# Kernel optimization log

Measured on AMD Instinct MI355X. Metric: run time of the kernel, lower is better.

The kernel has to match this reference:

```python
import jax, jax.numpy as jnp
import numpy as np
import math

B, T, C, H = 4, 2048, 1024, 16
D = C // H  # head dim = 64


def setup_inputs() -> dict:
    key = jax.random.key(0)
    ks = jax.random.split(key, 5)
    scale = 0.02
    x = jax.random.normal(ks[0], (B, T, C), dtype=jnp.float32)
    # torch nn.Linear(n_embd, 3*n_embd): weight [3C, C]; we store transposed [C, 3C]
    W_kqv = jax.random.normal(ks[1], (C, 3 * C), dtype=jnp.float32) * scale
    b_kqv = jnp.zeros((3 * C,), dtype=jnp.float32)
    W_proj = jax.random.normal(ks[2], (C, C), dtype=jnp.float32) * scale
    b_proj = jnp.zeros((C,), dtype=jnp.float32)
    padding_mask = jnp.ones((B, T), dtype=jnp.int32)  # 1 = valid token
    return {"x": x, "W_kqv": W_kqv, "b_kqv": b_kqv, "W_proj": W_proj,
            "b_proj": b_proj, "padding_mask": padding_mask}


def reference(x, W_kqv, b_kqv, W_proj, b_proj, padding_mask):
    Bx, Tx, Cx = x.shape
    kqv = x @ W_kqv + b_kqv                      # [B,T,3C]
    # original splits as k, q, v (in that order)
    k, q, v = jnp.split(kqv, 3, axis=2)
    def heads(t):
        return t.reshape(Bx, Tx, H, D).transpose(0, 2, 1, 3)  # [B,H,T,D]
    k, q, v = heads(k), heads(q), heads(v)
    att = jnp.einsum('bhqd,bhkd->bhqk', q, k) * (1.0 / math.sqrt(D))  # [B,H,T,T]
    causal = jnp.tril(jnp.ones((Tx, Tx), dtype=bool))[None, None]     # [1,1,T,T]
    valid = causal & (padding_mask[:, None, None, :] != 0)            # [B,1,T,T] broadcast
    neg_inf = jnp.finfo(att.dtype).min
    att = jnp.where(valid, att, neg_inf)
    att = jax.nn.softmax(att, axis=-1)
    y = jnp.einsum('bhqk,bhkd->bhqd', att, v)    # [B,H,T,D]
    y = y.transpose(0, 2, 1, 3).reshape(Bx, Tx, Cx)
    return y @ W_proj + b_proj
```

## Files before the change

### kernel.cpp

```cpp
#include <hip/hip_runtime.h>


typedef short bf16x8 __attribute__((ext_vector_type(8)));
typedef float floatx4 __attribute__((ext_vector_type(4)));

#define MFMA16(a, b, c) __builtin_amdgcn_mfma_f32_16x16x32_bf16(a, b, c, 0, 0, 0)

#define ASYNC_COPY16(gp, lp)                                                   \
  __builtin_amdgcn_global_load_lds(                                            \
      (__attribute__((address_space(1))) void*)(gp),                           \
      (__attribute__((address_space(3))) void*)(lp), 16, 0, 0)

#define DRAIN_VMCNT() asm volatile("s_waitcnt vmcnt(0)" ::: "memory")
#define WAIT_VMCNT6() asm volatile("s_waitcnt vmcnt(6)" ::: "memory")

#if defined(__has_builtin)
#if __has_builtin(__builtin_amdgcn_exp2f)
#define EXP2(x) __builtin_amdgcn_exp2f(x)
#endif
#endif
#ifndef EXP2
#define EXP2(x) exp2f(x)
#endif

__device__ __forceinline__ short f2bf(float f) {
  union { float f; unsigned u; } c;
  c.f = f;
  unsigned r = c.u + 0x7fffu + ((c.u >> 16) & 1u);
  return (short)(r >> 16);
}

__global__ __launch_bounds__(256) void cvt_f32_bf16(const float* __restrict__ in,
                                                    short* __restrict__ out) {
  int i = (blockIdx.x * 256 + threadIdx.x) * 4;
  float4 v = *(const float4*)&in[i];
  short4 o;
  o.x = f2bf(v.x); o.y = f2bf(v.y); o.z = f2bf(v.z); o.w = f2bf(v.w);
  *(short4*)&out[i] = o;
}

__global__ __launch_bounds__(256) void pmb_kernel(const int* __restrict__ pm,
                                                  float* __restrict__ pmbf) {
  int i = blockIdx.x * 256 + threadIdx.x;
  pmbf[i] = pm[i] ? 0.0f : -3.0e38f;
}

__global__ __launch_bounds__(256) void transpose_cvt_tiled(const float* __restrict__ in,
                                                           short* __restrict__ out,
                                                           int N) {
  __shared__ float buf[64][65];
  const int t = threadIdx.x;
  const int k0 = blockIdx.y * 64, n0 = blockIdx.x * 64;
#pragma unroll
  for (int i = 0; i < 4; ++i) {
    int s = t + i * 256;
    int row = s >> 4, c4 = (s & 15) * 4;
    float4 v = *(const float4*)&in[(size_t)(k0 + row) * N + n0 + c4];
    buf[row][c4] = v.x; buf[row][c4 + 1] = v.y;
    buf[row][c4 + 2] = v.z; buf[row][c4 + 3] = v.w;
  }
  __syncthreads();
#pragma unroll
  for (int i = 0; i < 2; ++i) {
    int u = t + i * 256;
    int rn = u >> 3, ch = (u & 7) * 8;
    short tmp[8];
#pragma unroll
    for (int j = 0; j < 8; ++j) tmp[j] = f2bf(buf[ch + j][rn]);
    *(uint4*)&out[(size_t)(n0 + rn) * 1024 + k0 + ch] = *(uint4*)tmp;
  }
}

template <int MODE>
__global__ __launch_bounds__(512, 2) void gemm_ph256(const short* __restrict__ A,
                                                     const short* __restrict__ Bt,
                                                     const float* __restrict__ bias,
                                                     void* __restrict__ Cout,
                                                     int M, int N, int K) {
  __shared__ short smem[73728];
  const int tid = threadIdx.x;
  const int lane = tid & 63;
  const int wv = tid >> 6;
  const int l15 = lane & 15, quad = lane >> 4;
  const int xr = l15 & 7;
  const int m0 = blockIdx.y * 128, n0 = blockIdx.x * 256;
  const int wm = (wv >> 2) * 64, wn = (wv & 3) * 64;
  const int NT = K >> 6;

  floatx4 acc[4][4] = {};

#define STAGE_A(kt, bs, j)                                                     \
  { int c_ = (j) * 512 + tid;                                                  \
    int r_ = c_ >> 3, ch_ = (c_ & 7) ^ (r_ & 7);                               \
    ASYNC_COPY16(&A[(size_t)(m0 + r_) * K + (kt) * 64 + ch_ * 8],              \
                 &smem[(bs) * 8192 + c_ * 8]); }
#define STAGE_B(kt, bs, j)                                                     \
  { int c_ = (j) * 512 + tid;                                                  \
    int r_ = c_ >> 3, ch_ = (c_ & 7) ^ (r_ & 7);                               \
    ASYNC_COPY16(&Bt[(size_t)(n0 + r_) * K + (kt) * 64 + ch_ * 8],             \
                 &smem[24576 + (bs) * 16384 + c_ * 8]); }

  STAGE_A(0, 0, 0); STAGE_A(0, 0, 1);
  STAGE_B(0, 0, 0); STAGE_B(0, 0, 1); STAGE_B(0, 0, 2); STAGE_B(0, 0, 3);
  STAGE_A(1, 1, 0); STAGE_A(1, 1, 1);
  STAGE_B(1, 1, 0); STAGE_B(1, 1, 1); STAGE_B(1, 1, 2); STAGE_B(1, 1, 3);
  WAIT_VMCNT6();
  __builtin_amdgcn_s_barrier();

  int cur = 0, nxt = 2;
  for (int kt = 0; kt < NT; ++kt) {
    const bool st = (kt + 2 < NT);
    const short* Asr = &smem[cur * 8192];
    const short* Bsr = &smem[24576 + cur * 16384];

    if (st) { STAGE_A(kt + 2, nxt, 0); STAGE_A(kt + 2, nxt, 1); STAGE_B(kt + 2, nxt, 0); }
    bf16x8 af[4][2], bf0[2][2];
#pragma unroll
    for (int mi = 0; mi < 4; ++mi)
#pragma unroll
      for (int s = 0; s < 2; ++s)
        af[mi][s] = *(const bf16x8*)
            &Asr[(wm + mi * 16 + l15) * 64 + (((s * 4 + quad) ^ xr) * 8)];
#pragma unroll
    for (int nj = 0; nj < 2; ++nj)
#pragma unroll
      for (int s = 0; s < 2; ++s)
        bf0[nj][s] = *(const bf16x8*)
            &Bsr[(wn + nj * 16 + l15) * 64 + (((s * 4 + quad) ^ xr) * 8)];
    __builtin_amdgcn_s_setprio(1);
#pragma unroll
    for (int s = 0; s < 2; ++s)
#pragma unroll
      for (int mi = 0; mi < 4; ++mi)
#pragma unroll
        for (int nj = 0; nj < 2; ++nj)
          acc[mi][nj] = MFMA16(af[mi][s], bf0[nj][s], acc[mi][nj]);
    __builtin_amdgcn_s_setprio(0);
    __builtin_amdgcn_s_barrier();

    if (st) { STAGE_B(kt + 2, nxt, 1); STAGE_B(kt + 2, nxt, 2); STAGE_B(kt + 2, nxt, 3); }
    bf16x8 bf1[2][2];
#pragma unroll
    for (int nj = 0; nj < 2; ++nj)
#pragma unroll
      for (int s = 0; s < 2; ++s)
        bf1[nj][s] = *(const bf16x8*)
            &Bsr[(wn + (2 + nj) * 16 + l15) * 64 + (((s * 4 + quad) ^ xr) * 8)];
    __builtin_amdgcn_s_setprio(1);
#pragma unroll
    for (int s = 0; s < 2; ++s)
#pragma unroll
      for (int mi = 0; mi < 4; ++mi)
#pragma unroll
        for (int nj = 0; nj < 2; ++nj)
          acc[mi][2 + nj] = MFMA16(af[mi][s], bf1[nj][s], acc[mi][2 + nj]);
    __builtin_amdgcn_s_setprio(0);
    if (st) { WAIT_VMCNT6(); } else { DRAIN_VMCNT(); }
    __builtin_amdgcn_s_barrier();
    cur = (cur == 2) ? 0 : cur + 1;
    nxt = (nxt == 2) ? 0 : nxt + 1;
  }
#undef STAGE_A
#undef STAGE_B

  if (MODE == 0) {
    float* outf = (float*)Cout;
#pragma unroll
    for (int ni = 0; ni < 4; ++ni) {
      int col = n0 + wn + ni * 16 + l15;
      float bv = bias[col];
#pragma unroll
      for (int mi = 0; mi < 4; ++mi) {
#pragma unroll
        for (int rr = 0; rr < 4; ++rr) {
          int row = m0 + wm + mi * 16 + quad * 4 + rr;
          outf[(size_t)row * N + col] = acc[mi][ni][rr] + bv;
        }
      }
    }
  } else {
    short* outs = (short*)Cout;
    const size_t QOFF = (size_t)64 * 2048 * 64;
    const int sec = n0 >> 10;
    short* Es = smem;
    if (sec < 2) {
#pragma unroll
      for (int ni = 0; ni < 4; ++ni) {
        int c = wn + ni * 16 + l15;
        float bv = bias[n0 + c];
#pragma unroll
        for (int mi = 0; mi < 4; ++mi) {
          int r0 = wm + mi * 16 + quad * 4;
#pragma unroll
          for (int rr = 0; rr < 4; ++rr) {
            int r = r0 + rr;
            Es[r * 256 + (c ^ (((r >> 2) & 3) << 4))] = f2bf(acc[mi][ni][rr] + bv);
          }
        }
      }
    } else {
#pragma unroll
      for (int ni = 0; ni < 4; ++ni) {
        int c = wn + ni * 16 + l15;
        float bv = bias[n0 + c];
#pragma unroll
        for (int mi = 0; mi < 4; ++mi) {
          int r0 = wm + mi * 16 + quad * 4;
#pragma unroll
          for (int rr = 0; rr < 4; ++rr) {
            int r = r0 + rr;
            Es[c * 128 + (r ^ ((c & 7) << 3))] = f2bf(acc[mi][ni][rr] + bv);
          }
        }
      }
    }
    __syncthreads();
    if (sec < 2) {
#pragma unroll
      for (int jj = 0; jj < 8; ++jj) {
        int idx = jj * 512 + tid;
        int rr2 = idx >> 5;
        int cc2 = (idx & 31) * 8;
        uint4 v = *(const uint4*)&Es[rr2 * 256 + (cc2 ^ (((rr2 >> 2) & 3) << 4))];
        int colg = n0 + cc2;
        int hh = (colg >> 6) & 15, dd = colg & 63;
        int row = m0 + rr2, bb = row >> 11, tt = row & 2047;
        *(uint4*)(outs + (size_t)sec * QOFF +
                  (((size_t)(bb * 16 + hh) * 2048 + tt) * 64 + dd)) = v;
      }
    } else {
#pragma unroll
      for (int jj = 0; jj < 8; ++jj) {
        int idx = jj * 512 + tid;
        int cd = idx >> 4;
        int rb = (idx & 15) * 8;
        uint4 v = *(const uint4*)&Es[cd * 128 + (rb ^ ((cd & 7) << 3))];
        int colg = n0 + cd;
        int hh = (colg >> 6) & 15, dd = colg & 63;
        int trow = m0 + rb, bb = trow >> 11, tt = trow & 2047;
        *(uint4*)(outs + 2 * QOFF +
                  ((size_t)(bb * 16 + hh) * 64 + dd) * 2048 + tt) = v;
      }
    }
  }
}

__global__ __launch_bounds__(256, 3) void attn_flash8(const short* __restrict__ Qd,
                                                      const short* __restrict__ Kd,
                                                      const short* __restrict__ Vd,
                                                      const float* __restrict__ pmbf,
                                                      short* __restrict__ y) {
  constexpr int T = 2048, C = 1024;
  __shared__ short Ks[2][64 * 64];
  __shared__ short Vs[2][64 * 64];
  __shared__ short Ps[4][32][64];

  const int tid = threadIdx.x;
  const int lane = tid & 63, w = tid >> 6;
  const int l15 = lane & 15, quad = lane >> 4;
  const int xr = l15 & 7;
  const int lin = blockIdx.x;
  const int qb = 15 - (lin >> 6);
  const int bh = lin & 63;
  const int b = bh >> 4, h = bh & 15;
  const short* Qb = Qd + (size_t)bh * T * 64;
  const short* Kb = Kd + (size_t)bh * T * 64;
  const short* Vb = Vd + (size_t)bh * 64 * T;
  const float* pmb = &pmbf[b * T];
  const int q0 = qb * 128;
  const int nt = (q0 >> 6) + 2;

  const float SCALE2 = 0.18033688011112042f;

#define STAGE_KV(t, buf)                                                       \
  {                                                                            \
    const short* ksrc_ = Kb + (size_t)((t) * 64) * 64;                         \
    const short* vsrc_ = Vb + (t) * 64;                                        \
    _Pragma("unroll")                                                          \
    for (int j_ = 0; j_ < 2; ++j_) {                                           \
      int c_ = j_ * 256 + tid;                                                 \
      int r_ = c_ >> 3, cc_ = (c_ & 7) ^ (r_ & 7);                             \
      ASYNC_COPY16(ksrc_ + r_ * 64 + cc_ * 8, &Ks[buf][c_ * 8]);               \
      ASYNC_COPY16(vsrc_ + (size_t)r_ * T + cc_ * 8, &Vs[buf][c_ * 8]);        \
    }                                                                          \
  }

  bf16x8 qf[2][2];
#pragma unroll
  for (int mi = 0; mi < 2; ++mi) {
    const short* qp = Qb + (size_t)(q0 + w * 32 + mi * 16 + l15) * 64;
    qf[mi][0] = *(const bf16x8*)&qp[quad * 8];
    qf[mi][1] = *(const bf16x8*)&qp[32 + quad * 8];
  }

  floatx4 Oacc[2][4] = {};
  float lpart[2] = {};

  STAGE_KV(0, 0);
  DRAIN_VMCNT();
  __syncthreads();

  int cur = 0;
#pragma unroll 1
  for (int t = 0; t < nt; ++t) {
    const int k0 = t * 64;
    if (t + 1 < nt) STAGE_KV(t + 1, cur ^ 1);

    floatx4 Sacc[2][4] = {};
#pragma unroll
    for (int s = 0; s < 2; ++s) {
#pragma unroll
      for (int n4 = 0; n4 < 4; ++n4) {
        bf16x8 bK = *(const bf16x8*)
            &Ks[cur][(n4 * 16 + l15) * 64 + (((s * 4 + quad) ^ xr) * 8)];
        Sacc[0][n4] = MFMA16(bK, qf[0][s], Sacc[0][n4]);
        Sacc[1][n4] = MFMA16(bK, qf[1][s], Sacc[1][n4]);
      }
    }

    if (k0 < q0) {
#pragma unroll
      for (int n4 = 0; n4 < 4; ++n4) {
        floatx4 pb4 = *(const floatx4*)&pmb[k0 + n4 * 16 + quad * 4];
#pragma unroll
        for (int mi = 0; mi < 2; ++mi) {
          float p[4];
#pragma unroll
          for (int rr = 0; rr < 4; ++rr) {
            p[rr] = EXP2(fmaf(Sacc[mi][n4][rr], SCALE2, pb4[rr]));
            lpart[mi] += p[rr];
          }
          unsigned lo, hi;
          asm("v_cvt_pk_bf16_f32 %0, %1, %2" : "=v"(lo) : "v"(p[0]), "v"(p[1]));
          asm("v_cvt_pk_bf16_f32 %0, %1, %2" : "=v"(hi) : "v"(p[2]), "v"(p[3]));
          uint2 pk; pk.x = lo; pk.y = hi;
          *(uint2*)&Ps[w][mi * 16 + l15]
                      [((n4 * 2 + (quad >> 1)) ^ xr) * 8 + (quad & 1) * 4] = pk;
        }
      }
    } else {
#pragma unroll
      for (int n4 = 0; n4 < 4; ++n4) {
        floatx4 pb4 = *(const floatx4*)&pmb[k0 + n4 * 16 + quad * 4];
        const int colb = n4 * 16 + quad * 4;
#pragma unroll
        for (int mi = 0; mi < 2; ++mi) {
          const int rowb = (q0 - k0) + w * 32 + mi * 16 + l15;
          float p[4];
#pragma unroll
          for (int rr = 0; rr < 4; ++rr) {
            float v = EXP2(fmaf(Sacc[mi][n4][rr], SCALE2, pb4[rr]));
            if (colb + rr > rowb) v = 0.f;
            p[rr] = v;
            lpart[mi] += v;
          }
          unsigned lo, hi;
          asm("v_cvt_pk_bf16_f32 %0, %1, %2" : "=v"(lo) : "v"(p[0]), "v"(p[1]));
          asm("v_cvt_pk_bf16_f32 %0, %1, %2" : "=v"(hi) : "v"(p[2]), "v"(p[3]));
          uint2 pk; pk.x = lo; pk.y = hi;
          *(uint2*)&Ps[w][mi * 16 + l15]
                      [((n4 * 2 + (quad >> 1)) ^ xr) * 8 + (quad & 1) * 4] = pk;
        }
      }
    }

#pragma unroll
    for (int ks2 = 0; ks2 < 2; ++ks2) {
      const int pco = (((ks2 * 4 + quad) ^ xr) * 8);
      bf16x8 ap0 = *(const bf16x8*)&Ps[w][l15][pco];
      bf16x8 ap1 = *(const bf16x8*)&Ps[w][16 + l15][pco];
#pragma unroll
      for (int nd = 0; nd < 4; ++nd) {
        bf16x8 bV = *(const bf16x8*)
            &Vs[cur][(nd * 16 + l15) * 64 + (((ks2 * 4 + quad) ^ xr) * 8)];
        Oacc[0][nd] = MFMA16(ap0, bV, Oacc[0][nd]);
        Oacc[1][nd] = MFMA16(ap1, bV, Oacc[1][nd]);
      }
    }

    DRAIN_VMCNT();
    __syncthreads();
    cur ^= 1;
  }
#undef STAGE_KV

#pragma unroll
  for (int mi = 0; mi < 2; ++mi) {
    float s = lpart[mi];
    s += __shfl_xor(s, 16, 64);
    s += __shfl_xor(s, 32, 64);
    float inv_l[4];
#pragma unroll
    for (int rr = 0; rr < 4; ++rr)
      inv_l[rr] = 1.0f / __shfl(s, quad * 4 + rr, 16);
#pragma unroll
    for (int n = 0; n < 4; ++n) {
      int dcol = n * 16 + l15;
#pragma unroll
      for (int rr = 0; rr < 4; ++rr) {
        int rowq = q0 + w * 32 + mi * 16 + quad * 4 + rr;
        y[((size_t)(b * T + rowq)) * C + h * 64 + dcol] =
            f2bf(Oacc[mi][n][rr] * inv_l[rr]);
      }
    }
  }
}

extern "C" void kernel_launch(void* const* d_in, const int* in_sizes, int n_in,
                              void* d_out, int out_size, void* d_ws, size_t ws_size,
                              hipStream_t stream) {
  constexpr int B = 4, T = 2048, C = 1024;
  constexpr int M = B * T;
  constexpr int N1 = 3 * C;

  const float* x      = (const float*)d_in[0];
  const float* W_kqv  = (const float*)d_in[1];
  const float* b_kqv  = (const float*)d_in[2];
  const float* W_proj = (const float*)d_in[3];
  const float* b_proj = (const float*)d_in[4];
  const int*   pmask  = (const int*)d_in[5];
  float* out = (float*)d_out;

  const size_t QOFF = (size_t)64 * T * 64;

  short* xb     = (short*)d_ws;
  short* Wkqvt  = xb + (size_t)M * C;
  short* Wprojt = Wkqvt + (size_t)N1 * C;
  short* qkv    = Wprojt + (size_t)C * C;
  float* pmbf   = (float*)(qkv + 3 * QOFF);
  short* yb     = xb;

  short* Kd = qkv;
  short* Qd = qkv + QOFF;
  short* Vd = qkv + 2 * QOFF;

  cvt_f32_bf16<<<(M * C) / (256 * 4), 256, 0, stream>>>(x, xb);
  transpose_cvt_tiled<<<dim3(N1 / 64, 16), 256, 0, stream>>>(W_kqv, Wkqvt, N1);
  transpose_cvt_tiled<<<dim3(C / 64, 16), 256, 0, stream>>>(W_proj, Wprojt, C);
  pmb_kernel<<<(B * T) / 256, 256, 0, stream>>>(pmask, pmbf);

  gemm_ph256<2><<<dim3(N1 / 256, M / 128), 512, 0, stream>>>(xb, Wkqvt, b_kqv, Kd, M, N1, C);

  attn_flash8<<<dim3(1024), 256, 0, stream>>>(Qd, Kd, Vd, pmbf, yb);

  gemm_ph256<0><<<dim3(C / 256, M / 128), 512, 0, stream>>>(yb, Wprojt, b_proj, out, M, C, C);
}
```

Baseline: 252.6 us.

## Split GEMM k-step into four quadrant phases and fuse prep kernels

```diff
diff --git a/kernel.cpp b/kernel.cpp
--- a/kernel.cpp
+++ b/kernel.cpp
@@ -39,18 +39,19 @@
   *(short4*)&out[i] = o;
 }
 
-__global__ __launch_bounds__(256) void pmb_kernel(const int* __restrict__ pm,
-                                                  float* __restrict__ pmbf) {
-  int i = blockIdx.x * 256 + threadIdx.x;
-  pmbf[i] = pm[i] ? 0.0f : -3.0e38f;
-}
-
-__global__ __launch_bounds__(256) void transpose_cvt_tiled(const float* __restrict__ in,
-                                                           short* __restrict__ out,
-                                                           int N) {
+__global__ __launch_bounds__(256) void transpose_cvt2(const float* __restrict__ inA,
+                                                      short* __restrict__ outA,
+                                                      const float* __restrict__ inB,
+                                                      short* __restrict__ outB) {
   __shared__ float buf[64][65];
   const int t = threadIdx.x;
-  const int k0 = blockIdx.y * 64, n0 = blockIdx.x * 64;
+  const int bx = blockIdx.x;
+  const float* in;
+  short* out;
+  int N, n0;
+  if (bx < 48) { in = inA; out = outA; N = 3072; n0 = bx * 64; }
+  else         { in = inB; out = outB; N = 1024; n0 = (bx - 48) * 64; }
+  const int k0 = blockIdx.y * 64;
 #pragma unroll
   for (int i = 0; i < 4; ++i) {
     int s = t + i * 256;
@@ -112,48 +113,77 @@
     const bool st = (kt + 2 < NT);
     const short* Asr = &smem[cur * 8192];
     const short* Bsr = &smem[24576 + cur * 16384];
-
-    if (st) { STAGE_A(kt + 2, nxt, 0); STAGE_A(kt + 2, nxt, 1); STAGE_B(kt + 2, nxt, 0); }
-    bf16x8 af[4][2], bf0[2][2];
-#pragma unroll
-    for (int mi = 0; mi < 4; ++mi)
+    bf16x8 aA[2][2], aB[2][2], bA[2][2], bB[2][2];
+
+    if (st) { STAGE_A(kt + 2, nxt, 0); STAGE_A(kt + 2, nxt, 1); }
+#pragma unroll
+    for (int mi = 0; mi < 2; ++mi)
 #pragma unroll
       for (int s = 0; s < 2; ++s)
-        af[mi][s] = *(const bf16x8*)
+        aA[mi][s] = *(const bf16x8*)
             &Asr[(wm + mi * 16 + l15) * 64 + (((s * 4 + quad) ^ xr) * 8)];
 #pragma unroll
     for (int nj = 0; nj < 2; ++nj)
 #pragma unroll
       for (int s = 0; s < 2; ++s)
-        bf0[nj][s] = *(const bf16x8*)
+        bA[nj][s] = *(const bf16x8*)
             &Bsr[(wn + nj * 16 + l15) * 64 + (((s * 4 + quad) ^ xr) * 8)];
     __builtin_amdgcn_s_setprio(1);
 #pragma unroll
     for (int s = 0; s < 2; ++s)
 #pragma unroll
-      for (int mi = 0; mi < 4; ++mi)
+      for (int mi = 0; mi < 2; ++mi)
 #pragma unroll
         for (int nj = 0; nj < 2; ++nj)
-          acc[mi][nj] = MFMA16(af[mi][s], bf0[nj][s], acc[mi][nj]);
+          acc[mi][nj] = MFMA16(aA[mi][s], bA[nj][s], acc[mi][nj]);
     __builtin_amdgcn_s_setprio(0);
     __builtin_amdgcn_s_barrier();
 
-    if (st) { STAGE_B(kt + 2, nxt, 1); STAGE_B(kt + 2, nxt, 2); STAGE_B(kt + 2, nxt, 3); }
-    bf16x8 bf1[2][2];
+    if (st) { STAGE_B(kt + 2, nxt, 0); STAGE_B(kt + 2, nxt, 1); }
+#pragma unroll
+    for (int mi = 0; mi < 2; ++mi)
+#pragma unroll
+      for (int s = 0; s < 2; ++s)
+        aB[mi][s] = *(const bf16x8*)
+            &Asr[(wm + (2 + mi) * 16 + l15) * 64 + (((s * 4 + quad) ^ xr) * 8)];
+    __builtin_amdgcn_s_setprio(1);
+#pragma unroll
+    for (int s = 0; s < 2; ++s)
+#pragma unroll
+      for (int mi = 0; mi < 2; ++mi)
+#pragma unroll
+        for (int nj = 0; nj < 2; ++nj)
+          acc[2 + mi][nj] = MFMA16(aB[mi][s], bA[nj][s], acc[2 + mi][nj]);
+    __builtin_amdgcn_s_setprio(0);
+    __builtin_amdgcn_s_barrier();
+
+    if (st) { STAGE_B(kt + 2, nxt, 2); }
 #pragma unroll
     for (int nj = 0; nj < 2; ++nj)
 #pragma unroll
       for (int s = 0; s < 2; ++s)
-        bf1[nj][s] = *(const bf16x8*)
+        bB[nj][s] = *(const bf16x8*)
             &Bsr[(wn + (2 + nj) * 16 + l15) * 64 + (((s * 4 + quad) ^ xr) * 8)];
     __builtin_amdgcn_s_setprio(1);
 #pragma unroll
     for (int s = 0; s < 2; ++s)
 #pragma unroll
-      for (int mi = 0; mi < 4; ++mi)
+      for (int mi = 0; mi < 2; ++mi)
 #pragma unroll
         for (int nj = 0; nj < 2; ++nj)
-          acc[mi][2 + nj] = MFMA16(af[mi][s], bf1[nj][s], acc[mi][2 + nj]);
+          acc[mi][2 + nj] = MFMA16(aA[mi][s], bB[nj][s], acc[mi][2 + nj]);
+    __builtin_amdgcn_s_setprio(0);
+    __builtin_amdgcn_s_barrier();
+
+    if (st) { STAGE_B(kt + 2, nxt, 3); }
+    __builtin_amdgcn_s_setprio(1);
+#pragma unroll
+    for (int s = 0; s < 2; ++s)
+#pragma unroll
+      for (int mi = 0; mi < 2; ++mi)
+#pragma unroll
+        for (int nj = 0; nj < 2; ++nj)
+          acc[2 + mi][2 + nj] = MFMA16(aB[mi][s], bB[nj][s], acc[2 + mi][2 + nj]);
     __builtin_amdgcn_s_setprio(0);
     if (st) { WAIT_VMCNT6(); } else { DRAIN_VMCNT(); }
     __builtin_amdgcn_s_barrier();
@@ -248,7 +278,7 @@
 __global__ __launch_bounds__(256, 3) void attn_flash8(const short* __restrict__ Qd,
                                                       const short* __restrict__ Kd,
                                                       const short* __restrict__ Vd,
-                                                      const float* __restrict__ pmbf,
+                                                      const int* __restrict__ pmask,
                                                       short* __restrict__ y) {
   constexpr int T = 2048, C = 1024;
   __shared__ short Ks[2][64 * 64];
@@ -266,7 +296,7 @@
   const short* Qb = Qd + (size_t)bh * T * 64;
   const short* Kb = Kd + (size_t)bh * T * 64;
   const short* Vb = Vd + (size_t)bh * 64 * T;
-  const float* pmb = &pmbf[b * T];
+  const int* pmi = &pmask[b * T];
   const int q0 = qb * 128;
   const int nt = (q0 >> 6) + 2;
 
@@ -321,13 +351,18 @@
     if (k0 < q0) {
 #pragma unroll
       for (int n4 = 0; n4 < 4; ++n4) {
-        floatx4 pb4 = *(const floatx4*)&pmb[k0 + n4 * 16 + quad * 4];
+        int4 pm4 = *(const int4*)&pmi[k0 + n4 * 16 + quad * 4];
+        float pb[4];
+        pb[0] = pm4.x ? 0.0f : -3.0e38f;
+        pb[1] = pm4.y ? 0.0f : -3.0e38f;
+        pb[2] = pm4.z ? 0.0f : -3.0e38f;
+        pb[3] = pm4.w ? 0.0f : -3.0e38f;
 #pragma unroll
         for (int mi = 0; mi < 2; ++mi) {
           float p[4];
 #pragma unroll
           for (int rr = 0; rr < 4; ++rr) {
-            p[rr] = EXP2(fmaf(Sacc[mi][n4][rr], SCALE2, pb4[rr]));
+            p[rr] = EXP2(fmaf(Sacc[mi][n4][rr], SCALE2, pb[rr]));
             lpart[mi] += p[rr];
           }
           unsigned lo, hi;
@@ -341,7 +376,12 @@
     } else {
 #pragma unroll
       for (int n4 = 0; n4 < 4; ++n4) {
-        floatx4 pb4 = *(const floatx4*)&pmb[k0 + n4 * 16 + quad * 4];
+        int4 pm4 = *(const int4*)&pmi[k0 + n4 * 16 + quad * 4];
+        float pb[4];
+        pb[0] = pm4.x ? 0.0f : -3.0e38f;
+        pb[1] = pm4.y ? 0.0f : -3.0e38f;
+        pb[2] = pm4.z ? 0.0f : -3.0e38f;
+        pb[3] = pm4.w ? 0.0f : -3.0e38f;
         const int colb = n4 * 16 + quad * 4;
 #pragma unroll
         for (int mi = 0; mi < 2; ++mi) {
@@ -349,7 +389,7 @@
           float p[4];
 #pragma unroll
           for (int rr = 0; rr < 4; ++rr) {
-            float v = EXP2(fmaf(Sacc[mi][n4][rr], SCALE2, pb4[rr]));
+            float v = EXP2(fmaf(Sacc[mi][n4][rr], SCALE2, pb[rr]));
             if (colb + rr > rowb) v = 0.f;
             p[rr] = v;
             lpart[mi] += v;
@@ -427,7 +467,6 @@
   short* Wkqvt  = xb + (size_t)M * C;
   short* Wprojt = Wkqvt + (size_t)N1 * C;
   short* qkv    = Wprojt + (size_t)C * C;
-  float* pmbf   = (float*)(qkv + 3 * QOFF);
   short* yb     = xb;
 
   short* Kd = qkv;
@@ -435,13 +474,11 @@
   short* Vd = qkv + 2 * QOFF;
 
   cvt_f32_bf16<<<(M * C) / (256 * 4), 256, 0, stream>>>(x, xb);
-  transpose_cvt_tiled<<<dim3(N1 / 64, 16), 256, 0, stream>>>(W_kqv, Wkqvt, N1);
-  transpose_cvt_tiled<<<dim3(C / 64, 16), 256, 0, stream>>>(W_proj, Wprojt, C);
-  pmb_kernel<<<(B * T) / 256, 256, 0, stream>>>(pmask, pmbf);
+  transpose_cvt2<<<dim3(64, 16), 256, 0, stream>>>(W_kqv, Wkqvt, W_proj, Wprojt);
 
   gemm_ph256<2><<<dim3(N1 / 256, M / 128), 512, 0, stream>>>(xb, Wkqvt, b_kqv, Kd, M, N1, C);
 
-  attn_flash8<<<dim3(1024), 256, 0, stream>>>(Qd, Kd, Vd, pmbf, yb);
+  attn_flash8<<<dim3(1024), 256, 0, stream>>>(Qd, Kd, Vd, pmask, yb);
 
   gemm_ph256<0><<<dim3(C / 256, M / 128), 512, 0, stream>>>(yb, Wprojt, b_proj, out, M, C, C);
 }
```

Measured after the change: 248.3 us. About the same (-1.7%).
